# Performance work log

Measured on AMD Instinct MI355X. Metric: run time of the kernel, lower is better.

Reference implementation:

```python
import jax, jax.numpy as jnp
import numpy as np

N, E, D, H = 50000, 800000, 64, 4  # nodes, edges, dim_embedding (=per-head channels), heads
NEG_SLOPE = 0.2
EPS = 1e-16


def _gat(x, src, dst, W, att_src, att_dst, bias, n):
    # x: [N, Din], W: [Din, H*D] -> per-head features [N, H, D]
    xw = (x @ W).reshape(n, H, D)
    a_src = jnp.einsum('nhc,hc->nh', xw, att_src)  # [N, H]
    a_dst = jnp.einsum('nhc,hc->nh', xw, att_dst)
    logits = jax.nn.leaky_relu(a_src[src] + a_dst[dst], NEG_SLOPE)  # [E, H]
    # segment softmax over incoming edges of each destination node
    m = jax.ops.segment_max(logits, dst, num_segments=n)  # [N, H]
    ex = jnp.exp(logits - m[dst])
    s = jax.ops.segment_sum(ex, dst, num_segments=n)
    alpha = ex / (s[dst] + EPS)  # [E, H]
    msg = xw[src] * alpha[..., None]  # [E, H, D]
    out = jax.ops.segment_sum(msg, dst, num_segments=n)  # [N, H, D]
    return out.mean(axis=1) + bias  # concat=False head-mean, [N, D]


def setup_inputs() -> dict:
    key = jax.random.key(0)
    ks = jax.random.split(key, 16)
    sc = 1.0 / np.sqrt(D)
    inp = {
        'x': jax.random.normal(ks[0], (N, D), jnp.float32),
        'edge_index': jax.random.randint(ks[1], (2, E), 0, N, jnp.int64),
    }
    for i, tag in ((2, '1'), (9, '2')):
        inp['W' + tag] = jax.random.normal(ks[i], (D, H * D), jnp.float32) * sc
        inp['att_src' + tag] = jax.random.normal(ks[i + 1], (H, D), jnp.float32) * sc
        inp['att_dst' + tag] = jax.random.normal(ks[i + 2], (H, D), jnp.float32) * sc
        inp['b' + tag] = jnp.zeros((D,), jnp.float32)
        inp['lW' + tag] = jax.random.normal(ks[i + 3], (D, D), jnp.float32) * sc
        inp['lb' + tag] = jnp.zeros((D,), jnp.float32)
    return inp


def reference(x, edge_index, W1, att_src1, att_dst1, b1, lW1, lb1,
              W2, att_src2, att_dst2, b2, lW2, lb2):
    src, dst = edge_index[0], edge_index[1]
    n = x.shape[0]
    h = _gat(x, src, dst, W1, att_src1, att_dst1, b1, n) + (x @ lW1 + lb1)
    h = jax.nn.relu(h)
    out = _gat(h, src, dst, W2, att_src2, att_dst2, b2, n) + (h @ lW2 + lb2)
    return out
```

## Files before the change

kernel.cpp:

```cpp
#include <hip/hip_runtime.h>
#include <math.h>

typedef __attribute__((ext_vector_type(8))) short short8;
typedef __attribute__((ext_vector_type(4))) float f32x4;
typedef __attribute__((ext_vector_type(4))) int i32x4;

__device__ inline unsigned fenc(float f){
  unsigned u = __float_as_uint(f);
  return u ^ ((u >> 31) ? 0xFFFFFFFFu : 0x80000000u);
}
__device__ inline float fdec(unsigned k){
  unsigned u = (k & 0x80000000u) ? (k ^ 0x80000000u) : ~k;
  return __uint_as_float(u);
}
__device__ inline unsigned short bf16rne(float f){
  unsigned u = __float_as_uint(f);
  return (unsigned short)((u + 0x7FFFu + ((u >> 16) & 1u)) >> 16);
}

__global__ __launch_bounds__(256) void k_hist(const int* __restrict__ dst, int* __restrict__ deg, int E){
  int e = blockIdx.x*256 + threadIdx.x;
  if (e < E) atomicAdd(&deg[dst[e]], 1);
}

__global__ __launch_bounds__(256) void k_scan_local(const int* __restrict__ deg, int* __restrict__ offs,
    int* __restrict__ blksum, int nelem, int ndeg){
  __shared__ int sh[256];
  int t = threadIdx.x;
  int i = blockIdx.x*256 + t;
  int v = (i < ndeg) ? deg[i] : 0;
  sh[t] = v; __syncthreads();
  for (int d = 1; d < 256; d <<= 1){
    int add = (t >= d) ? sh[t-d] : 0; __syncthreads();
    sh[t] += add; __syncthreads();
  }
  if (i < nelem) offs[i] = sh[t] - v;
  if (t == 255) blksum[blockIdx.x] = sh[t];
}

__global__ __launch_bounds__(256) void k_scan_blk(int* __restrict__ blksum, int nb){
  __shared__ int sh[256];
  int t = threadIdx.x;
  int running = 0;
  for (int base = 0; base < nb; base += 256){
    int v = (base+t < nb) ? blksum[base+t] : 0;
    __syncthreads();
    sh[t] = v; __syncthreads();
    for (int d = 1; d < 256; d <<= 1){
      int add = (t >= d) ? sh[t-d] : 0; __syncthreads();
      sh[t] += add; __syncthreads();
    }
    if (base+t < nb) blksum[base+t] = running + sh[t] - v;
    running += sh[255];
  }
}

__global__ __launch_bounds__(256) void k_scan_add(int* __restrict__ offs, const int* __restrict__ blksum, int nelem){
  int i = blockIdx.x*256 + threadIdx.x;
  if (i < nelem) offs[i] += blksum[blockIdx.x];
}

__global__ __launch_bounds__(512) void k_prep(
    const float* __restrict__ W1, const float* __restrict__ as1, const float* __restrict__ ad1,
    const float* __restrict__ b1, const float* __restrict__ lb1, const float* __restrict__ lW1,
    const float* __restrict__ W2, const float* __restrict__ as2, const float* __restrict__ ad2,
    const float* __restrict__ b2, const float* __restrict__ lb2, const float* __restrict__ lW2,
    short* __restrict__ wbigT, short* __restrict__ wattBsw, float* __restrict__ bcomb,
    unsigned* __restrict__ gmax, int4* __restrict__ rec, int E){
  int L = blockIdx.x;
  const float* W   = L ? W2  : W1;
  const float* asv = L ? as2 : as1;
  const float* adv = L ? ad2 : ad1;
  const float* b   = L ? b2  : b1;
  const float* lb  = L ? lb2 : lb1;
  const float* lW  = L ? lW2 : lW1;
  short* wbT = wbigT  + (size_t)L*64*328;
  short* wsw = wattBsw + L*1024;
  float* bc  = bcomb  + L*64;
  __shared__ float watt[512];
  int t = threadIdx.x;
  { int j = t >> 6, k = t & 63, h = j & 3;
    const float* att = (j < 4) ? asv : adv;
    float s = 0.f;
    for (int c = 0; c < 64; ++c) s += W[k*256 + h*64 + c] * att[h*64 + c];
    watt[j*64 + k] = s; }
  if (t < 8) gmax[t] = 0u;
  if (t < 64) bc[t] = b[t] + lb[t];
  if (L == 0 && t < 16){ int4 z; z.x = 0; z.y = 0; z.z = 0; z.w = 0; rec[E + t] = z; }
  __syncthreads();
  for (int i = t; i < 1024; i += 512){
    int step = i >> 9, lane = (i >> 3) & 63, j = i & 7;
    int col = lane & 15, q = lane >> 4, k = step*32 + q*8 + j;
    float v = (col < 8) ? watt[col*64 + k] : 0.f;
    wsw[i] = (short)bf16rne(v);
  }
  for (int i = t; i < 64*328; i += 512){
    int c = i / 328, q = i - c*328;
    float val = 0.f;
    if (q < 256){ int hh = q >> 6, cin = q & 63; val = 0.25f * W[cin*256 + hh*64 + c]; }
    else if (q < 320){ int kk = q - 256; val = lW[kk*64 + c]; }
    wbT[i] = (short)bf16rne(val);
  }
}

__global__ __launch_bounds__(256) void k_att(const float* __restrict__ featF,
    const unsigned short* __restrict__ featB, const short* __restrict__ wattBsw,
    float* __restrict__ asrc, float* __restrict__ adst, unsigned short* __restrict__ xbf,
    unsigned* __restrict__ gmax, int n){
  __shared__ unsigned shm[4];
  int t = threadIdx.x;
  if (t < 4) shm[t] = 0u;
  __syncthreads();
  int lane = t & 63, w = t >> 6;
  int nodebase = blockIdx.x*64 + w*16;
  int row16 = lane & 15, q = lane >> 4;
  int rowc = nodebase + row16; if (rowc > n-1) rowc = n-1;
  short8 a0, a1;
  if (featF){
    const float* fp = featF + (size_t)rowc*64;
    float4 c00 = *(const float4*)(fp + q*8);
    float4 c01 = *(const float4*)(fp + q*8 + 4);
    float4 c10 = *(const float4*)(fp + 32 + q*8);
    float4 c11 = *(const float4*)(fp + 32 + q*8 + 4);
    a0[0]=(short)bf16rne(c00.x); a0[1]=(short)bf16rne(c00.y); a0[2]=(short)bf16rne(c00.z); a0[3]=(short)bf16rne(c00.w);
    a0[4]=(short)bf16rne(c01.x); a0[5]=(short)bf16rne(c01.y); a0[6]=(short)bf16rne(c01.z); a0[7]=(short)bf16rne(c01.w);
    a1[0]=(short)bf16rne(c10.x); a1[1]=(short)bf16rne(c10.y); a1[2]=(short)bf16rne(c10.z); a1[3]=(short)bf16rne(c10.w);
    a1[4]=(short)bf16rne(c11.x); a1[5]=(short)bf16rne(c11.y); a1[6]=(short)bf16rne(c11.z); a1[7]=(short)bf16rne(c11.w);
    *(short8*)(xbf + (size_t)rowc*64 + q*8) = a0;
    *(short8*)(xbf + (size_t)rowc*64 + 32 + q*8) = a1;
  } else {
    a0 = *(const short8*)(featB + (size_t)rowc*64 + q*8);
    a1 = *(const short8*)(featB + (size_t)rowc*64 + 32 + q*8);
  }
  short8 b0 = *(const short8*)(wattBsw + lane*8);
  short8 b1 = *(const short8*)(wattBsw + 512 + lane*8);
  f32x4 acc = {0.f,0.f,0.f,0.f};
  acc = __builtin_amdgcn_mfma_f32_16x16x32_bf16(a0, b0, acc, 0, 0, 0);
  acc = __builtin_amdgcn_mfma_f32_16x16x32_bf16(a1, b1, acc, 0, 0, 0);
  int c = lane & 15;
  int rbase = nodebase + q*4;
  if (c < 8){
    float* dstp = (c < 4) ? asrc : adst;
    int hh = c & 3;
    float vmax = -INFINITY;
    #pragma unroll
    for (int r = 0; r < 4; ++r){
      int rr = rbase + r; if (rr > n-1) rr = n-1;
      dstp[(size_t)rr*4 + hh] = acc[r];
      vmax = fmaxf(vmax, acc[r]);
    }
    if (c < 4) atomicMax(&shm[hh], fenc(vmax));
  }
  __syncthreads();
  if (t < 4) atomicMax(gmax + t, shm[t]);
}

__global__ __launch_bounds__(256) void k_scatedge(const int* __restrict__ src, const int* __restrict__ dst,
    const float* __restrict__ asrc, const float* __restrict__ adst,
    const int* __restrict__ offs, int* __restrict__ cursor, const unsigned* __restrict__ gmax,
    int4* __restrict__ rec, int E){
  int e = blockIdx.x*256 + threadIdx.x;
  if (e >= E) return;
  int s = src[e], d = dst[e];
  float4 as = *(const float4*)(asrc + (size_t)s*4);
  float4 ad = *(const float4*)(adst + (size_t)d*4);
  float g0 = fdec(gmax[0]) + ad.x; g0 = fmaxf(g0, 0.2f*g0);
  float g1 = fdec(gmax[1]) + ad.y; g1 = fmaxf(g1, 0.2f*g1);
  float g2 = fdec(gmax[2]) + ad.z; g2 = fmaxf(g2, 0.2f*g2);
  float g3 = fdec(gmax[3]) + ad.w; g3 = fmaxf(g3, 0.2f*g3);
  float l0 = as.x + ad.x; l0 = fmaxf(l0, 0.2f*l0);
  float l1 = as.y + ad.y; l1 = fmaxf(l1, 0.2f*l1);
  float l2 = as.z + ad.z; l2 = fmaxf(l2, 0.2f*l2);
  float l3 = as.w + ad.w; l3 = fmaxf(l3, 0.2f*l3);
  unsigned lo = (unsigned)bf16rne(__expf(l0 - g0)) | ((unsigned)bf16rne(__expf(l1 - g1)) << 16);
  unsigned hi = (unsigned)bf16rne(__expf(l2 - g2)) | ((unsigned)bf16rne(__expf(l3 - g3)) << 16);
  int pos = offs[d] + atomicAdd(&cursor[d], 1);
  i32x4 r; r.x = (int)lo; r.y = (int)hi; r.z = s; r.w = d;
  __builtin_nontemporal_store(r, (i32x4*)(rec + pos));
}

__global__ __launch_bounds__(256) void k_edge2(int4* __restrict__ rec,
    const float* __restrict__ asrc, const float* __restrict__ adst,
    const unsigned* __restrict__ gmax, int E){
  int i = blockIdx.x*256 + threadIdx.x;
  if (i >= E) return;
  int4 r = rec[i];
  int s = r.z, d = r.w;
  float4 as = *(const float4*)(asrc + (size_t)s*4);
  float4 ad = *(const float4*)(adst + (size_t)d*4);
  float g0 = fdec(gmax[0]) + ad.x; g0 = fmaxf(g0, 0.2f*g0);
  float g1 = fdec(gmax[1]) + ad.y; g1 = fmaxf(g1, 0.2f*g1);
  float g2 = fdec(gmax[2]) + ad.z; g2 = fmaxf(g2, 0.2f*g2);
  float g3 = fdec(gmax[3]) + ad.w; g3 = fmaxf(g3, 0.2f*g3);
  float l0 = as.x + ad.x; l0 = fmaxf(l0, 0.2f*l0);
  float l1 = as.y + ad.y; l1 = fmaxf(l1, 0.2f*l1);
  float l2 = as.z + ad.z; l2 = fmaxf(l2, 0.2f*l2);
  float l3 = as.w + ad.w; l3 = fmaxf(l3, 0.2f*l3);
  r.x = (int)((unsigned)bf16rne(__expf(l0 - g0)) | ((unsigned)bf16rne(__expf(l1 - g1)) << 16));
  r.y = (int)((unsigned)bf16rne(__expf(l2 - g2)) | ((unsigned)bf16rne(__expf(l3 - g3)) << 16));
  rec[i] = r;
}

__global__ __launch_bounds__(64) void k_agg(const int4* __restrict__ rec,
    const int* __restrict__ offs, const unsigned short* __restrict__ xbf,
    short* __restrict__ Abf, int n){
  int v = blockIdx.x;
  int lane = threadIdx.x & 63;
  int rs = __builtin_amdgcn_readfirstlane(offs[v]);
  int re = __builtin_amdgcn_readfirstlane(offs[v+1]);
  int nrem = re - rs;
  const int4* rp = rec + rs;
  float s0=0.f,s1=0.f,s2=0.f,s3=0.f;
  float a0=0.f,a1=0.f,a2=0.f,a3=0.f;

#define ACC(LO,HI,XU) { \
    float xc = __uint_as_float(((unsigned)(XU)) << 16); \
    float p0 = __uint_as_float((LO) << 16); \
    float p1 = __uint_as_float((LO) & 0xFFFF0000u); \
    float p2 = __uint_as_float((HI) << 16); \
    float p3 = __uint_as_float((HI) & 0xFFFF0000u); \
    s0 += p0; s1 += p1; s2 += p2; s3 += p3; \
    a0 = fmaf(p0, xc, a0); a1 = fmaf(p1, xc, a1); \
    a2 = fmaf(p2, xc, a2); a3 = fmaf(p3, xc, a3); }

  int nch = nrem >> 2;
  if (nch > 0){
    int4 R0[4], R1[4], T[4], U[4];
    unsigned xw0[4], xw1[4];
    #pragma unroll
    for (int j = 0; j < 4; ++j) R0[j] = rp[j];
    #pragma unroll
    for (int j = 0; j < 4; ++j) xw0[j] = xbf[(((size_t)(unsigned)R0[j].z)<<6)+lane];
    #pragma unroll
    for (int j = 0; j < 4; ++j) R1[j] = rp[4+j];
    int c = 0;
    for (; c + 1 < nch; c += 2){
      #pragma unroll
      for (int j = 0; j < 4; ++j) T[j] = rp[((c+2)<<2)+j];
      #pragma unroll
      for (int j = 0; j < 4; ++j) xw1[j] = xbf[(((size_t)(unsigned)R1[j].z)<<6)+lane];
      #pragma unroll
      for (int j = 0; j < 4; ++j) U[j] = rp[((c+3)<<2)+j];
      #pragma unroll
      for (int j = 0; j < 4; ++j) ACC((unsigned)R0[j].x, (unsigned)R0[j].y, xw0[j]);
      #pragma unroll
      for (int j = 0; j < 4; ++j) R0[j] = T[j];
      #pragma unroll
      for (int j = 0; j < 4; ++j) xw0[j] = xbf[(((size_t)(unsigned)R0[j].z)<<6)+lane];
      #pragma unroll
      for (int j = 0; j < 4; ++j) ACC((unsigned)R1[j].x, (unsigned)R1[j].y, xw1[j]);
      #pragma unroll
      for (int j = 0; j < 4; ++j) R1[j] = U[j];
    }
    if (c < nch){
      #pragma unroll
      for (int j = 0; j < 4; ++j) ACC((unsigned)R0[j].x, (unsigned)R0[j].y, xw0[j]);
    }
  }
  for (int i = nch<<2; i < nrem; ++i){
    int4 t = rp[i];
    unsigned xt = xbf[(((size_t)(unsigned)t.z)<<6)+lane];
    ACC((unsigned)t.x, (unsigned)t.y, xt);
  }
#undef ACC
  size_t base = (size_t)v*256 + lane;
  Abf[base +   0] = (short)bf16rne(a0 / (s0 + 1e-16f));
  Abf[base +  64] = (short)bf16rne(a1 / (s1 + 1e-16f));
  Abf[base + 128] = (short)bf16rne(a2 / (s2 + 1e-16f));
  Abf[base + 192] = (short)bf16rne(a3 / (s3 + 1e-16f));
}

__global__ __launch_bounds__(256) void k_out(const short* __restrict__ Abf,
    const unsigned short* __restrict__ xbf, const short* __restrict__ wbigT,
    const float* __restrict__ bcomb, float* __restrict__ outF, unsigned short* __restrict__ outB, int n){
  __shared__ __align__(16) short sB[64*328];
  {
    const short8* gs = (const short8*)wbigT;
    short8* ls = (short8*)sB;
    for (int i = threadIdx.x; i < 64*328/8; i += 256) ls[i] = gs[i];
  }
  __syncthreads();
  int lane = threadIdx.x & 63, wid = threadIdx.x >> 6;
  int rowbase = blockIdx.x*64 + wid*16;
  int arow = rowbase + (lane & 15); if (arow > n-1) arow = n-1;
  int ksub = (lane >> 4) * 8;
  const short* ap = Abf + (size_t)arow*256 + ksub;
  const short* xp = (const short*)xbf + (size_t)arow*64 + ksub;
  const short* bp = sB + (lane & 15)*328 + ksub;
  f32x4 acc0 = {0.f,0.f,0.f,0.f}, acc1 = acc0, acc2 = acc0, acc3 = acc0;
  #pragma unroll
  for (int k0 = 0; k0 < 320; k0 += 32){
    short8 a  = (k0 < 256) ? *(const short8*)(ap + k0) : *(const short8*)(xp + (k0 - 256));
    short8 b0 = *(const short8*)(bp + k0);
    short8 b1 = *(const short8*)(bp + 16*328 + k0);
    short8 b2 = *(const short8*)(bp + 32*328 + k0);
    short8 b3 = *(const short8*)(bp + 48*328 + k0);
    acc0 = __builtin_amdgcn_mfma_f32_16x16x32_bf16(a, b0, acc0, 0, 0, 0);
    acc1 = __builtin_amdgcn_mfma_f32_16x16x32_bf16(a, b1, acc1, 0, 0, 0);
    acc2 = __builtin_amdgcn_mfma_f32_16x16x32_bf16(a, b2, acc2, 0, 0, 0);
    acc3 = __builtin_amdgcn_mfma_f32_16x16x32_bf16(a, b3, acc3, 0, 0, 0);
  }
  int ccol = lane & 15;
  int crow = rowbase + (lane >> 4)*4;
  float bb0 = bcomb[ 0 + ccol];
  float bb1 = bcomb[16 + ccol];
  float bb2 = bcomb[32 + ccol];
  float bb3 = bcomb[48 + ccol];
  #pragma unroll
  for (int r = 0; r < 4; ++r){
    int rr = crow + r;
    if (rr < n){
      float o0 = acc0[r] + bb0, o1 = acc1[r] + bb1, o2 = acc2[r] + bb2, o3 = acc3[r] + bb3;
      if (outB){
        unsigned short* orow = outB + (size_t)rr*64;
        orow[ 0 + ccol] = bf16rne(fmaxf(o0, 0.f));
        orow[16 + ccol] = bf16rne(fmaxf(o1, 0.f));
        orow[32 + ccol] = bf16rne(fmaxf(o2, 0.f));
        orow[48 + ccol] = bf16rne(fmaxf(o3, 0.f));
      } else {
        float* orow = outF + (size_t)rr*64;
        orow[ 0 + ccol] = o0;
        orow[16 + ccol] = o1;
        orow[32 + ccol] = o2;
        orow[48 + ccol] = o3;
      }
    }
  }
}

extern "C" void kernel_launch(void* const* d_in, const int* in_sizes, int n_in,
                              void* d_out, int out_size, void* d_ws, size_t ws_size,
                              hipStream_t stream){
  const float* x   = (const float*)d_in[0];
  const int*   ei  = (const int*)d_in[1];
  const float* W1  = (const float*)d_in[2];
  const float* as1 = (const float*)d_in[3];
  const float* ad1 = (const float*)d_in[4];
  const float* b1  = (const float*)d_in[5];
  const float* lW1 = (const float*)d_in[6];
  const float* lb1 = (const float*)d_in[7];
  const float* W2  = (const float*)d_in[8];
  const float* as2 = (const float*)d_in[9];
  const float* ad2 = (const float*)d_in[10];
  const float* b2  = (const float*)d_in[11];
  const float* lW2 = (const float*)d_in[12];
  const float* lb2 = (const float*)d_in[13];
  int N = in_sizes[0] / 64;
  int E = in_sizes[1] / 2;
  const int* srce = ei;
  const int* dste = ei + E;

  char* w = (char*)d_ws;
  size_t off = 0;
  auto alloc = [&](size_t bytes)->char*{
    char* p = w + off; off = (off + bytes + 255) & ~(size_t)255; return p;
  };
  int*      offs    = (int*)     alloc((size_t)(N+1)*4);
  int*      deg     = (int*)     alloc((size_t)N*4);
  int*      cursor  = (int*)     alloc((size_t)N*4);
  int*      blksum  = (int*)     alloc(4096);
  int4*     rec     = (int4*)    alloc((size_t)(E+16)*16);
  short*    wbigT   = (short*)   alloc((size_t)2*64*328*2);
  short*    wattBsw = (short*)   alloc(2*1024*2);
  float*    bcomb   = (float*)   alloc(2*64*4);
  unsigned* gmax    = (unsigned*)alloc(32);
  float*    pasrc   = (float*)   alloc((size_t)N*16);
  float*    padst   = (float*)   alloc((size_t)N*16);
  short*    Abf     = (short*)   alloc((size_t)N*256*2);
  unsigned short* xbf1 = (unsigned short*)alloc((size_t)N*64*2);
  unsigned short* xbf2 = (unsigned short*)alloc((size_t)N*64*2);
  (void)ws_size; (void)n_in; (void)out_size;

  (void)hipMemsetAsync(deg, 0, (size_t)N*4, stream);
  (void)hipMemsetAsync(cursor, 0, (size_t)N*4, stream);

  int gE = (E + 255)/256;
  int nelem = N + 1;
  int nb = (nelem + 255)/256;
  int gATT = (N + 63)/64;
  int gOUT = (N + 63)/64;
  float* outp = (float*)d_out;

  k_prep<<<2, 512, 0, stream>>>(W1, as1, ad1, b1, lb1, lW1,
                                W2, as2, ad2, b2, lb2, lW2,
                                wbigT, wattBsw, bcomb, gmax, rec, E);

  k_hist<<<gE, 256, 0, stream>>>(dste, deg, E);
  k_scan_local<<<nb, 256, 0, stream>>>(deg, offs, blksum, nelem, N);
  k_scan_blk<<<1, 256, 0, stream>>>(blksum, nb);
  k_scan_add<<<nb, 256, 0, stream>>>(offs, blksum, nelem);

  k_att <<<gATT, 256, 0, stream>>>(x, nullptr, wattBsw, pasrc, padst, xbf1, gmax, N);
  k_scatedge<<<gE, 256, 0, stream>>>(srce, dste, pasrc, padst, offs, cursor, gmax, rec, E);
  k_agg <<<N, 64, 0, stream>>>(rec, offs, xbf1, Abf, N);
  k_out <<<gOUT, 256, 0, stream>>>(Abf, xbf1, wbigT, bcomb, nullptr, xbf2, N);

  k_att <<<gATT, 256, 0, stream>>>(nullptr, xbf2, wattBsw + 1024, pasrc, padst, nullptr, gmax + 4, N);
  k_edge2<<<gE, 256, 0, stream>>>(rec, pasrc, padst, gmax + 4, E);
  k_agg <<<N, 64, 0, stream>>>(rec, offs, xbf2, Abf, N);
  k_out <<<gOUT, 256, 0, stream>>>(Abf, xbf2, wbigT + 64*328, bcomb + 64, outp, nullptr, N);
}
```

Baseline: 240.0 us.

## Partition edge scatter by destination range per XCD using ticketed persistent blocks

Turns the edge-scatter kernel into a persistent grid of 1024 blocks. Each block reads its XCD id from a hardware register and first works on the destination-node range matching that XCD, taking slices of edges through atomic tickets. The aim is to keep the cursor atomics and record writes for a given destination range inside one XCD's L2, cutting cross-die traffic. The cost is that every block rescans dst for all 8 ranges, so each edge's dst is read up to 8 times, plus ticket synchronisation overhead. It also drops the nontemporal store on records.

```diff
diff --git a/kernel.cpp b/kernel.cpp
--- a/kernel.cpp
+++ b/kernel.cpp
@@ -3,7 +3,6 @@
 
 typedef __attribute__((ext_vector_type(8))) short short8;
 typedef __attribute__((ext_vector_type(4))) float f32x4;
-typedef __attribute__((ext_vector_type(4))) int i32x4;
 
 __device__ inline unsigned fenc(float f){
   unsigned u = __float_as_uint(f);
@@ -66,7 +65,7 @@
     const float* __restrict__ W2, const float* __restrict__ as2, const float* __restrict__ ad2,
     const float* __restrict__ b2, const float* __restrict__ lb2, const float* __restrict__ lW2,
     short* __restrict__ wbigT, short* __restrict__ wattBsw, float* __restrict__ bcomb,
-    unsigned* __restrict__ gmax, int4* __restrict__ rec, int E){
+    unsigned* __restrict__ gmax, int* __restrict__ tickets, int4* __restrict__ rec, int E){
   int L = blockIdx.x;
   const float* W   = L ? W2  : W1;
   const float* asv = L ? as2 : as1;
@@ -85,6 +84,7 @@
     for (int c = 0; c < 64; ++c) s += W[k*256 + h*64 + c] * att[h*64 + c];
     watt[j*64 + k] = s; }
   if (t < 8) gmax[t] = 0u;
+  if (L == 0 && t < 8) tickets[t] = 0;
   if (t < 64) bc[t] = b[t] + lb[t];
   if (L == 0 && t < 16){ int4 z; z.x = 0; z.y = 0; z.z = 0; z.w = 0; rec[E + t] = z; }
   __syncthreads();
@@ -155,28 +155,51 @@
   if (t < 4) atomicMax(gmax + t, shm[t]);
 }
 
+#define SLICE 4096
 __global__ __launch_bounds__(256) void k_scatedge(const int* __restrict__ src, const int* __restrict__ dst,
     const float* __restrict__ asrc, const float* __restrict__ adst,
     const int* __restrict__ offs, int* __restrict__ cursor, const unsigned* __restrict__ gmax,
-    int4* __restrict__ rec, int E){
-  int e = blockIdx.x*256 + threadIdx.x;
-  if (e >= E) return;
-  int s = src[e], d = dst[e];
-  float4 as = *(const float4*)(asrc + (size_t)s*4);
-  float4 ad = *(const float4*)(adst + (size_t)d*4);
-  float g0 = fdec(gmax[0]) + ad.x; g0 = fmaxf(g0, 0.2f*g0);
-  float g1 = fdec(gmax[1]) + ad.y; g1 = fmaxf(g1, 0.2f*g1);
-  float g2 = fdec(gmax[2]) + ad.z; g2 = fmaxf(g2, 0.2f*g2);
-  float g3 = fdec(gmax[3]) + ad.w; g3 = fmaxf(g3, 0.2f*g3);
-  float l0 = as.x + ad.x; l0 = fmaxf(l0, 0.2f*l0);
-  float l1 = as.y + ad.y; l1 = fmaxf(l1, 0.2f*l1);
-  float l2 = as.z + ad.z; l2 = fmaxf(l2, 0.2f*l2);
-  float l3 = as.w + ad.w; l3 = fmaxf(l3, 0.2f*l3);
-  unsigned lo = (unsigned)bf16rne(__expf(l0 - g0)) | ((unsigned)bf16rne(__expf(l1 - g1)) << 16);
-  unsigned hi = (unsigned)bf16rne(__expf(l2 - g2)) | ((unsigned)bf16rne(__expf(l3 - g3)) << 16);
-  int pos = offs[d] + atomicAdd(&cursor[d], 1);
-  i32x4 r; r.x = (int)lo; r.y = (int)hi; r.z = s; r.w = d;
-  __builtin_nontemporal_store(r, (i32x4*)(rec + pos));
+    int4* __restrict__ rec, int E, int nslices, unsigned rmag, int* __restrict__ tickets){
+  __shared__ int sh_s;
+  unsigned myx = __builtin_amdgcn_s_getreg((31u<<11) | 20u) & 7u;
+  float gm0 = fdec(gmax[0]), gm1 = fdec(gmax[1]), gm2 = fdec(gmax[2]), gm3 = fdec(gmax[3]);
+  int t = threadIdx.x;
+  for (unsigned rr = 0; rr < 8; ++rr){
+    unsigned r = (myx + rr) & 7u;
+    while (true){
+      __syncthreads();
+      if (t == 0) sh_s = atomicAdd(&tickets[r], 1);
+      __syncthreads();
+      int s = sh_s;
+      if (s >= nslices) break;
+      int base = s * SLICE + t;
+      #pragma unroll
+      for (int k = 0; k < SLICE/256; ++k){
+        int e = base + k*256;
+        if (e < E){
+          int d = __builtin_nontemporal_load(dst + e);
+          if (__umulhi((unsigned)d, rmag) == r){
+            int sid = __builtin_nontemporal_load(src + e);
+            float4 as = *(const float4*)(asrc + (size_t)sid*4);
+            float4 ad = *(const float4*)(adst + (size_t)d*4);
+            float g0 = gm0 + ad.x; g0 = fmaxf(g0, 0.2f*g0);
+            float g1 = gm1 + ad.y; g1 = fmaxf(g1, 0.2f*g1);
+            float g2 = gm2 + ad.z; g2 = fmaxf(g2, 0.2f*g2);
+            float g3 = gm3 + ad.w; g3 = fmaxf(g3, 0.2f*g3);
+            float l0 = as.x + ad.x; l0 = fmaxf(l0, 0.2f*l0);
+            float l1 = as.y + ad.y; l1 = fmaxf(l1, 0.2f*l1);
+            float l2 = as.z + ad.z; l2 = fmaxf(l2, 0.2f*l2);
+            float l3 = as.w + ad.w; l3 = fmaxf(l3, 0.2f*l3);
+            unsigned lo = (unsigned)bf16rne(__expf(l0 - g0)) | ((unsigned)bf16rne(__expf(l1 - g1)) << 16);
+            unsigned hi = (unsigned)bf16rne(__expf(l2 - g2)) | ((unsigned)bf16rne(__expf(l3 - g3)) << 16);
+            int pos = offs[d] + atomicAdd(&cursor[d], 1);
+            int4 rv; rv.x = (int)lo; rv.y = (int)hi; rv.z = sid; rv.w = d;
+            rec[pos] = rv;
+          }
+        }
+      }
+    }
+  }
 }
 
 __global__ __launch_bounds__(256) void k_edge2(int4* __restrict__ rec,
@@ -359,6 +382,7 @@
   int*      deg     = (int*)     alloc((size_t)N*4);
   int*      cursor  = (int*)     alloc((size_t)N*4);
   int*      blksum  = (int*)     alloc(4096);
+  int*      tickets = (int*)     alloc(32);
   int4*     rec     = (int4*)    alloc((size_t)(E+16)*16);
   short*    wbigT   = (short*)   alloc((size_t)2*64*328*2);
   short*    wattBsw = (short*)   alloc(2*1024*2);
@@ -379,11 +403,13 @@
   int nb = (nelem + 255)/256;
   int gATT = (N + 63)/64;
   int gOUT = (N + 63)/64;
+  int nslices = (E + SLICE - 1)/SLICE;
+  unsigned rmag = (unsigned)(((unsigned long long)8 << 32) / (unsigned)N);
   float* outp = (float*)d_out;
 
   k_prep<<<2, 512, 0, stream>>>(W1, as1, ad1, b1, lb1, lW1,
                                 W2, as2, ad2, b2, lb2, lW2,
-                                wbigT, wattBsw, bcomb, gmax, rec, E);
+                                wbigT, wattBsw, bcomb, gmax, tickets, rec, E);
 
   k_hist<<<gE, 256, 0, stream>>>(dste, deg, E);
   k_scan_local<<<nb, 256, 0, stream>>>(deg, offs, blksum, nelem, N);
@@ -391,7 +417,8 @@
   k_scan_add<<<nb, 256, 0, stream>>>(offs, blksum, nelem);
 
   k_att <<<gATT, 256, 0, stream>>>(x, nullptr, wattBsw, pasrc, padst, xbf1, gmax, N);
-  k_scatedge<<<gE, 256, 0, stream>>>(srce, dste, pasrc, padst, offs, cursor, gmax, rec, E);
+  k_scatedge<<<1024, 256, 0, stream>>>(srce, dste, pasrc, padst, offs, cursor, gmax, rec,
+                                       E, nslices, rmag, tickets);
   k_agg <<<N, 64, 0, stream>>>(rec, offs, xbf1, Abf, N);
   k_out <<<gOUT, 256, 0, stream>>>(Abf, xbf1, wbigT, bcomb, nullptr, xbf2, N);
 
```

After: 336.0 us. +40.0%, slower.
